# Kernel optimization log

Hardware: AMD Instinct MI355X
Metric: run time of the kernel (lower is better)

The kernel has to match this reference:

```python
import jax, jax.numpy as jnp
import numpy as np

B, S, C, H, D = 4, 2048, 512, 8, 64
EPS = 1e-5
SCALE = D ** -0.5


def layer_norm(x, w, b):
    m = jnp.mean(x, axis=-1, keepdims=True)
    v = jnp.var(x, axis=-1, keepdims=True)
    return (x - m) * jax.lax.rsqrt(v + EPS) * w + b


def setup_inputs() -> dict:
    key = jax.random.key(0)
    ks = jax.random.split(key, 7)
    s = 0.02
    return {
        "x": jax.random.normal(ks[0], (B, S, C), jnp.float32),
        "Wq": jax.random.normal(ks[1], (C, H * D), jnp.float32) * s,
        "Wk": jax.random.normal(ks[2], (C, H * D), jnp.float32) * s,
        "Wv": jax.random.normal(ks[3], (C, H * D), jnp.float32) * s,
        "Wo": jax.random.normal(ks[4], (H * D, C), jnp.float32) * s,
        "ln1_w": jnp.ones((C,), jnp.float32), "ln1_b": jnp.zeros((C,), jnp.float32),
        "ff_ln1_w": jnp.ones((C,), jnp.float32), "ff_ln1_b": jnp.zeros((C,), jnp.float32),
        "ff_w1": jax.random.normal(ks[5], (C, C), jnp.float32) * s, "ff_b1": jnp.zeros((C,), jnp.float32),
        "ff_ln2_w": jnp.ones((C,), jnp.float32), "ff_ln2_b": jnp.zeros((C,), jnp.float32),
        "ff_w2": jax.random.normal(ks[6], (C, C), jnp.float32) * s, "ff_b2": jnp.zeros((C,), jnp.float32),
        "ln2_w": jnp.ones((C,), jnp.float32), "ln2_b": jnp.zeros((C,), jnp.float32),
    }


def causal_attention(x, Wq, Wk, Wv, Wo):
    # Mathematically identical to the bucketed memory-efficient attention:
    # online-softmax bucketing changes compute order, not the result.
    q = (x @ Wq).reshape(B, S, H, D).transpose(0, 2, 1, 3)  # [B,H,S,D]
    k = (x @ Wk).reshape(B, S, H, D).transpose(0, 2, 1, 3)
    v = (x @ Wv).reshape(B, S, H, D).transpose(0, 2, 1, 3)
    scores = jnp.einsum('bhqd,bhkd->bhqk', q, k) * SCALE  # [B,H,S,S]
    causal = jnp.tril(jnp.ones((S, S), bool))
    scores = jnp.where(causal, scores, jnp.finfo(scores.dtype).min)
    attn = jax.nn.softmax(scores, axis=-1)
    out = jnp.einsum('bhqk,bhkd->bhqd', attn, v)
    out = out.transpose(0, 2, 1, 3).reshape(B, S, H * D)
    return out @ Wo


def reference(x, Wq, Wk, Wv, Wo, ln1_w, ln1_b, ff_ln1_w, ff_ln1_b, ff_w1, ff_b1,
              ff_ln2_w, ff_ln2_b, ff_w2, ff_b2, ln2_w, ln2_b):
    a = causal_attention(x, Wq, Wk, Wv, Wo)
    x_ln = layer_norm(a + x, ln1_w, ln1_b)
    h = layer_norm(x_ln, ff_ln1_w, ff_ln1_b) @ ff_w1 + ff_b1
    h = layer_norm(h, ff_ln2_w, ff_ln2_b) @ ff_w2 + ff_b2
    return layer_norm(h + x_ln, ln2_w, ln2_b)
```

## Files before the change

### kernel.cpp

```cpp
#include <hip/hip_runtime.h>

#define B_ 4
#define S_ 2048
#define C_ 512
#define H_ 8
#define D_ 64
#define M_ 8192

typedef short s8v __attribute__((ext_vector_type(8)));
typedef short s4v __attribute__((ext_vector_type(4)));
typedef float f4v __attribute__((ext_vector_type(4)));
typedef unsigned short u16;
typedef unsigned int u32;

__device__ __forceinline__ u16 f2b(float f) {
    u32 u = __builtin_bit_cast(u32, f);
    u = u + 0x7fffu + ((u >> 16) & 1u);
    return (u16)(u >> 16);
}

__device__ __forceinline__ void b2f8(const s8v v, float* f) {
    #pragma unroll
    for (int k = 0; k < 8; ++k)
        f[k] = __builtin_bit_cast(float, (u32)(u16)v[k] << 16);
}

__device__ __forceinline__ void gl2lds16(const void* g, void* l) {
    __builtin_amdgcn_global_load_lds(
        (const __attribute__((address_space(1))) void*)g,
        (__attribute__((address_space(3))) void*)l, 16, 0, 0);
}

__global__ __launch_bounds__(256) void prep_k(const float* __restrict__ x,
                                              u16* __restrict__ xb,
                                              const float* __restrict__ s0,
                                              const float* __restrict__ s1,
                                              const float* __restrict__ s2,
                                              const float* __restrict__ s3,
                                              const float* __restrict__ s4,
                                              const float* __restrict__ s5,
                                              u16* __restrict__ d0,
                                              u16* __restrict__ d1,
                                              u16* __restrict__ d2,
                                              u16* __restrict__ d3,
                                              u16* __restrict__ d4,
                                              u16* __restrict__ d5)
{
    __shared__ float t[32][33];
    const int bx = blockIdx.x;
    if (bx < 4096) {
        const int i = (bx * 256 + (int)threadIdx.x) * 4;
        const float4 v = *(const float4*)&x[i];
        ushort4 o;
        o.x = f2b(v.x); o.y = f2b(v.y); o.z = f2b(v.z); o.w = f2b(v.w);
        *(ushort4*)&xb[i] = o;
        return;
    }
    const int tb = bx - 4096;
    const int z = tb >> 8, rem = tb & 255;
    const float* W; u16* Wt;
    switch (z) {
        case 0: W = s0; Wt = d0; break;
        case 1: W = s1; Wt = d1; break;
        case 2: W = s2; Wt = d2; break;
        case 3: W = s3; Wt = d3; break;
        case 4: W = s4; Wt = d4; break;
        default: W = s5; Wt = d5; break;
    }
    const int tx = threadIdx.x & 31, ty = threadIdx.x >> 5;
    const int n0 = (rem & 15) * 32, k0 = (rem >> 4) * 32;
    #pragma unroll
    for (int i = 0; i < 4; ++i)
        t[ty + i * 8][tx] = W[(size_t)(k0 + ty + i * 8) * C_ + n0 + tx];
    __syncthreads();
    #pragma unroll
    for (int i = 0; i < 4; ++i)
        Wt[(size_t)(n0 + ty + i * 8) * C_ + k0 + tx] = f2b(t[tx][ty + i * 8]);
}

template <bool OB>
__global__ __launch_bounds__(256) void gemm_k(const u16* __restrict__ A,
                                              const u16* __restrict__ Bt,
                                              const float* __restrict__ bias,
                                              void* __restrict__ outv)
{
    __shared__ u16 As[2][128][64];
    __shared__ u16 Bs[2][64][64];
    const int tid = threadIdx.x;
    const int lane = tid & 63, w = tid >> 6;
    const int q4 = lane >> 4, l16 = lane & 15;
    const int wr = w >> 1, wc = w & 1;
    const int bm = blockIdx.x * 128, bn = blockIdx.y * 64;
    const int sr8  = lane >> 3;
    const int scol = ((lane & 7) ^ sr8) * 8;

    f4v acc[4][2];
    #pragma unroll
    for (int i = 0; i < 4; ++i)
        #pragma unroll
        for (int j = 0; j < 2; ++j) acc[i][j] = (f4v){0.f, 0.f, 0.f, 0.f};

    const u16* Ab = A  + (size_t)bm * C_;
    const u16* Bb = Bt + (size_t)bn * C_;

    auto stage = [&](int bf, int kt) {
        const int k0 = kt * 64;
        #pragma unroll
        for (int t = 0; t < 4; ++t)
            gl2lds16(Ab + (size_t)(w * 32 + t * 8 + sr8) * C_ + k0 + scol,
                     (char*)As + bf * 16384 + (w * 32 + t * 8) * 128);
        #pragma unroll
        for (int t = 0; t < 2; ++t)
            gl2lds16(Bb + (size_t)(w * 16 + t * 8 + sr8) * C_ + k0 + scol,
                     (char*)Bs + bf * 8192 + (w * 16 + t * 8) * 128);
    };

    stage(0, 0);
    for (int kt = 0; kt < 8; ++kt) {
        __syncthreads();
        const int bf = kt & 1;
        if (kt < 7) stage(bf ^ 1, kt + 1);
        #pragma unroll
        for (int kk = 0; kk < 2; ++kk) {
            const int pc = ((kk * 4 + q4) ^ (l16 & 7)) * 8;
            s8v a[4], b[2];
            #pragma unroll
            for (int i = 0; i < 4; ++i)
                a[i] = *(const s8v*)&As[bf][wr * 64 + i * 16 + l16][pc];
            #pragma unroll
            for (int j = 0; j < 2; ++j)
                b[j] = *(const s8v*)&Bs[bf][wc * 32 + j * 16 + l16][pc];
            #pragma unroll
            for (int i = 0; i < 4; ++i)
                #pragma unroll
                for (int j = 0; j < 2; ++j)
                    acc[i][j] = __builtin_amdgcn_mfma_f32_16x16x32_bf16(a[i], b[j], acc[i][j], 0, 0, 0);
        }
    }

    #pragma unroll
    for (int j = 0; j < 2; ++j) {
        const int n = bn + wc * 32 + j * 16 + l16;
        const float bj = bias ? bias[n] : 0.0f;
        #pragma unroll
        for (int i = 0; i < 4; ++i) {
            const int m = bm + wr * 64 + i * 16 + q4 * 4;
            #pragma unroll
            for (int reg = 0; reg < 4; ++reg) {
                const float vv = acc[i][j][reg] + bj;
                if constexpr (OB) ((u16*)outv)[(size_t)(m + reg) * C_ + n] = f2b(vv);
                else              ((float*)outv)[(size_t)(m + reg) * C_ + n] = vv;
            }
        }
    }
}

__global__ __launch_bounds__(256) void qkv_k(const u16* __restrict__ A,
                                             const u16* __restrict__ Wq,
                                             const u16* __restrict__ Wk,
                                             const u16* __restrict__ Wv,
                                             u16* __restrict__ oq,
                                             u16* __restrict__ ok,
                                             u16* __restrict__ ovt)
{
    __shared__ u16 As[2][128][64];
    __shared__ u16 Bs[2][64][64];
    const int tid = threadIdx.x;
    const int lane = tid & 63, w = tid >> 6;
    const int q4 = lane >> 4, l16 = lane & 15;
    const int wr = w >> 1, wc = w & 1;
    const int nt = blockIdx.y, which = nt >> 3;
    const u16* Bt = which == 0 ? Wq : (which == 1 ? Wk : Wv);
    const int bm = blockIdx.x * 128, bn = (nt & 7) * 64;
    const int sr8  = lane >> 3;
    const int scol = ((lane & 7) ^ sr8) * 8;

    f4v acc[4][2];
    #pragma unroll
    for (int i = 0; i < 4; ++i)
        #pragma unroll
        for (int j = 0; j < 2; ++j) acc[i][j] = (f4v){0.f, 0.f, 0.f, 0.f};

    const u16* Ab = A  + (size_t)bm * C_;
    const u16* Bb = Bt + (size_t)bn * C_;

    auto stage = [&](int bf, int kt) {
        const int k0 = kt * 64;
        #pragma unroll
        for (int t = 0; t < 4; ++t)
            gl2lds16(Ab + (size_t)(w * 32 + t * 8 + sr8) * C_ + k0 + scol,
                     (char*)As + bf * 16384 + (w * 32 + t * 8) * 128);
        #pragma unroll
        for (int t = 0; t < 2; ++t)
            gl2lds16(Bb + (size_t)(w * 16 + t * 8 + sr8) * C_ + k0 + scol,
                     (char*)Bs + bf * 8192 + (w * 16 + t * 8) * 128);
    };

    stage(0, 0);
    for (int kt = 0; kt < 8; ++kt) {
        __syncthreads();
        const int bf = kt & 1;
        if (kt < 7) stage(bf ^ 1, kt + 1);
        #pragma unroll
        for (int kk = 0; kk < 2; ++kk) {
            const int pc = ((kk * 4 + q4) ^ (l16 & 7)) * 8;
            s8v a[4], b[2];
            #pragma unroll
            for (int i = 0; i < 4; ++i)
                a[i] = *(const s8v*)&As[bf][wr * 64 + i * 16 + l16][pc];
            #pragma unroll
            for (int j = 0; j < 2; ++j)
                b[j] = *(const s8v*)&Bs[bf][wc * 32 + j * 16 + l16][pc];
            #pragma unroll
            for (int i = 0; i < 4; ++i)
                #pragma unroll
                for (int j = 0; j < 2; ++j)
                    acc[i][j] = __builtin_amdgcn_mfma_f32_16x16x32_bf16(a[i], b[j], acc[i][j], 0, 0, 0);
        }
    }

    if (which == 0) {
        #pragma unroll
        for (int j = 0; j < 2; ++j) {
            const int n = bn + wc * 32 + j * 16 + l16;
            #pragma unroll
            for (int i = 0; i < 4; ++i) {
                const int m = bm + wr * 64 + i * 16 + q4 * 4;
                #pragma unroll
                for (int reg = 0; reg < 4; ++reg)
                    oq[(size_t)(m + reg) * C_ + n] = f2b(acc[i][j][reg]);
            }
        }
    } else if (which == 1) {
        #pragma unroll
        for (int j = 0; j < 2; ++j) {
            const int n = bn + wc * 32 + j * 16 + l16;
            const int nswz = (n & ~31) | ((((n >> 3) & 3) ^ q4) << 3) | (n & 7);
            #pragma unroll
            for (int i = 0; i < 4; ++i) {
                const int m = bm + wr * 64 + i * 16 + q4 * 4;
                #pragma unroll
                for (int reg = 0; reg < 4; ++reg)
                    ok[(size_t)(m + reg) * C_ + nswz] = f2b(acc[i][j][reg]);
            }
        }
    } else {
        const int bglob = bm >> 11;
        const int sbase = bm & (S_ - 1);
        #pragma unroll
        for (int j = 0; j < 2; ++j) {
            const int n = bn + wc * 32 + j * 16 + l16;
            const int h = n >> 6, d = n & 63;
            u16* vrow = ovt + ((size_t)(bglob * H_ + h) * D_ + d) * S_;
            const int xw = d & 7;
            #pragma unroll
            for (int i = 0; i < 4; ++i) {
                const int s = sbase + wr * 64 + i * 16 + q4 * 4;
                const int pg = ((s & 31) >> 2) ^ xw;
                s4v pv;
                #pragma unroll
                for (int reg = 0; reg < 4; ++reg) pv[reg] = (short)f2b(acc[i][j][reg]);
                *(s4v*)&vrow[(s & ~31) + (pg << 2)] = pv;
            }
        }
    }
}

__global__ __launch_bounds__(256) void ln2xb_k(const u16* __restrict__ in,
                                               const float* __restrict__ res,
                                               const float* __restrict__ w1,
                                               const float* __restrict__ b1,
                                               const float* __restrict__ w2,
                                               const float* __restrict__ b2,
                                               u16* __restrict__ out1,
                                               u16* __restrict__ out2)
{
    const int lane = threadIdx.x & 63;
    const int row  = blockIdx.x * 4 + (threadIdx.x >> 6);
    const size_t off = (size_t)row * C_ + lane * 8;
    float v[8];
    b2f8(*(const s8v*)&in[off], v);
    {
        const float4 r0 = *(const float4*)&res[off];
        const float4 r1 = *(const float4*)&res[off + 4];
        v[0] += r0.x; v[1] += r0.y; v[2] += r0.z; v[3] += r0.w;
        v[4] += r1.x; v[5] += r1.y; v[6] += r1.z; v[7] += r1.w;
    }
    float s = 0.f, ss = 0.f;
    #pragma unroll
    for (int k = 0; k < 8; ++k) { s += v[k]; ss += v[k] * v[k]; }
    #pragma unroll
    for (int o = 32; o >= 1; o >>= 1) { s += __shfl_xor(s, o); ss += __shfl_xor(ss, o); }
    float mean = s * (1.0f / C_);
    float rstd = rsqrtf(ss * (1.0f / C_) - mean * mean + 1e-5f);

    const float4 wA0 = *(const float4*)&w1[lane * 8];
    const float4 wA1 = *(const float4*)&w1[lane * 8 + 4];
    const float4 bA0 = *(const float4*)&b1[lane * 8];
    const float4 bA1 = *(const float4*)&b1[lane * 8 + 4];
    const float wA[8] = {wA0.x, wA0.y, wA0.z, wA0.w, wA1.x, wA1.y, wA1.z, wA1.w};
    const float bA[8] = {bA0.x, bA0.y, bA0.z, bA0.w, bA1.x, bA1.y, bA1.z, bA1.w};
    float y[8];
    s8v o1;
    #pragma unroll
    for (int k = 0; k < 8; ++k) {
        y[k] = (v[k] - mean) * rstd * wA[k] + bA[k];
        o1[k] = (short)f2b(y[k]);
    }
    *(s8v*)&out1[off] = o1;

    s = 0.f; ss = 0.f;
    #pragma unroll
    for (int k = 0; k < 8; ++k) { s += y[k]; ss += y[k] * y[k]; }
    #pragma unroll
    for (int o = 32; o >= 1; o >>= 1) { s += __shfl_xor(s, o); ss += __shfl_xor(ss, o); }
    mean = s * (1.0f / C_);
    rstd = rsqrtf(ss * (1.0f / C_) - mean * mean + 1e-5f);

    const float4 wB0 = *(const float4*)&w2[lane * 8];
    const float4 wB1 = *(const float4*)&w2[lane * 8 + 4];
    const float4 bB0 = *(const float4*)&b2[lane * 8];
    const float4 bB1 = *(const float4*)&b2[lane * 8 + 4];
    const float wB[8] = {wB0.x, wB0.y, wB0.z, wB0.w, wB1.x, wB1.y, wB1.z, wB1.w};
    const float bB[8] = {bB0.x, bB0.y, bB0.z, bB0.w, bB1.x, bB1.y, bB1.z, bB1.w};
    s8v o2;
    #pragma unroll
    for (int k = 0; k < 8; ++k)
        o2[k] = (short)f2b((y[k] - mean) * rstd * wB[k] + bB[k]);
    *(s8v*)&out2[off] = o2;
}

__global__ __launch_bounds__(256) void lnb_k(const u16* __restrict__ in,
                                             const float* __restrict__ w,
                                             const float* __restrict__ bb,
                                             u16* __restrict__ out)
{
    const int lane = threadIdx.x & 63;
    const int row  = blockIdx.x * 4 + (threadIdx.x >> 6);
    const size_t off = (size_t)row * C_ + lane * 8;
    float v[8];
    b2f8(*(const s8v*)&in[off], v);
    float s = 0.f, ss = 0.f;
    #pragma unroll
    for (int k = 0; k < 8; ++k) { s += v[k]; ss += v[k] * v[k]; }
    #pragma unroll
    for (int o = 32; o >= 1; o >>= 1) { s += __shfl_xor(s, o); ss += __shfl_xor(ss, o); }
    const float mean = s * (1.0f / C_);
    const float rstd = rsqrtf(ss * (1.0f / C_) - mean * mean + 1e-5f);
    const float4 w0 = *(const float4*)&w[lane * 8];
    const float4 w1 = *(const float4*)&w[lane * 8 + 4];
    const float4 b0 = *(const float4*)&bb[lane * 8];
    const float4 b1 = *(const float4*)&bb[lane * 8 + 4];
    const float wv[8] = {w0.x, w0.y, w0.z, w0.w, w1.x, w1.y, w1.z, w1.w};
    const float bv[8] = {b0.x, b0.y, b0.z, b0.w, b1.x, b1.y, b1.z, b1.w};
    s8v o;
    #pragma unroll
    for (int k = 0; k < 8; ++k)
        o[k] = (short)f2b((v[k] - mean) * rstd * wv[k] + bv[k]);
    *(s8v*)&out[off] = o;
}

__global__ __launch_bounds__(256) void lnfin_k(const u16* __restrict__ in,
                                               const u16* __restrict__ res,
                                               const float* __restrict__ w,
                                               const float* __restrict__ bb,
                                               float* __restrict__ out)
{
    const int lane = threadIdx.x & 63;
    const int row  = blockIdx.x * 4 + (threadIdx.x >> 6);
    const size_t off = (size_t)row * C_ + lane * 8;
    float v[8], r[8];
    b2f8(*(const s8v*)&in[off], v);
    b2f8(*(const s8v*)&res[off], r);
    #pragma unroll
    for (int k = 0; k < 8; ++k) v[k] += r[k];
    float s = 0.f, ss = 0.f;
    #pragma unroll
    for (int k = 0; k < 8; ++k) { s += v[k]; ss += v[k] * v[k]; }
    #pragma unroll
    for (int o = 32; o >= 1; o >>= 1) { s += __shfl_xor(s, o); ss += __shfl_xor(ss, o); }
    const float mean = s * (1.0f / C_);
    const float rstd = rsqrtf(ss * (1.0f / C_) - mean * mean + 1e-5f);
    const float4 w0 = *(const float4*)&w[lane * 8];
    const float4 w1 = *(const float4*)&w[lane * 8 + 4];
    const float4 b0 = *(const float4*)&bb[lane * 8];
    const float4 b1 = *(const float4*)&bb[lane * 8 + 4];
    const float wv[8] = {w0.x, w0.y, w0.z, w0.w, w1.x, w1.y, w1.z, w1.w};
    const float bv[8] = {b0.x, b0.y, b0.z, b0.w, b1.x, b1.y, b1.z, b1.w};
    float4 o0, o1;
    o0.x = (v[0] - mean) * rstd * wv[0] + bv[0];
    o0.y = (v[1] - mean) * rstd * wv[1] + bv[1];
    o0.z = (v[2] - mean) * rstd * wv[2] + bv[2];
    o0.w = (v[3] - mean) * rstd * wv[3] + bv[3];
    o1.x = (v[4] - mean) * rstd * wv[4] + bv[4];
    o1.y = (v[5] - mean) * rstd * wv[5] + bv[5];
    o1.z = (v[6] - mean) * rstd * wv[6] + bv[6];
    o1.w = (v[7] - mean) * rstd * wv[7] + bv[7];
    *(float4*)&out[off]     = o0;
    *(float4*)&out[off + 4] = o1;
}

__global__ __launch_bounds__(512, 4) void attn_k(const u16* __restrict__ Q,
                                                 const u16* __restrict__ K,
                                                 const u16* __restrict__ Vt,
                                                 u16* __restrict__ O)
{
    __shared__ char smem[65536];
    u16* KsB = (u16*)smem;
    u16* VsB = (u16*)(smem + 32768);
    const int tid = threadIdx.x;
    const int lane = tid & 63, w = tid >> 6;
    const int grp = w >> 2, wl = w & 3;
    const int q4 = lane >> 4, l16 = lane & 15;
    const int h = blockIdx.y, b = blockIdx.z;
    const int px = blockIdx.x;
    const int qH = 31 - px, qL = px;
    const int nH = 32 - px;
    const size_t base  = ((size_t)b * S_) * C_ + h * D_;
    const size_t basev = ((size_t)(b * H_ + h)) * D_ * S_;
    const int lr = lane >> 2, lc = (lane & 3) * 8;
    const int kq = (q4 ^ ((l16 >> 2) & 3)) * 8;
    const int qrow = wl * 16 + l16;

    auto stage = [&](int kb, int sl) {
        #pragma unroll
        for (int r = 0; r < 2; ++r) {
            const int seg = r * 4 + wl;
            const int row = (seg & 3) * 16 + lr;
            const int kh = seg >> 2;
            gl2lds16(K  + base  + (size_t)(kb * 64 + row) * C_ + kh * 32 + lc,
                     (char*)KsB + sl * 8192 + seg * 1024);
            gl2lds16(Vt + basev + (size_t)row * S_ + kb * 64 + kh * 32 + lc,
                     (char*)VsB + sl * 8192 + seg * 1024);
        }
    };

    s8v qf[2];
    #pragma unroll
    for (int kh = 0; kh < 2; ++kh)
        qf[kh] = *(const s8v*)&Q[base + (size_t)(qH * 64 + qrow) * C_ + kh * 32 + q4 * 8];

    f4v acc[4]; float lp[4];
    f4v oH[4];  float lpH[4];
    #pragma unroll
    for (int j = 0; j < 4; ++j) {
        acc[j] = (f4v){0.f, 0.f, 0.f, 0.f}; lp[j] = 0.f;
        oH[j]  = (f4v){0.f, 0.f, 0.f, 0.f}; lpH[j] = 0.f;
    }
    bool dumped = false;

    stage(grp, grp);

    for (int t = 0; t <= 16; ++t) {
        __syncthreads();
        const int s = 2 * t + grp;
        if (s <= 32) {
            const int s2 = s + 2;
            if (s2 <= 32) {
                const int kb2 = s2 < nH ? s2 : s2 - nH;
                stage(kb2, s2 & 3);
            }
            if (s >= nH && !dumped) {
                dumped = true;
                #pragma unroll
                for (int j = 0; j < 4; ++j) {
                    oH[j] = acc[j]; lpH[j] = lp[j];
                    acc[j] = (f4v){0.f, 0.f, 0.f, 0.f}; lp[j] = 0.f;
                }
                #pragma unroll
                for (int kh = 0; kh < 2; ++kh)
                    qf[kh] = *(const s8v*)&Q[base + (size_t)(qL * 64 + qrow) * C_ + kh * 32 + q4 * 8];
            }
            const int kb = s < nH ? s : s - nH;
            const int sl = s & 3;
            const u16* ks = KsB + sl * 4096;
            const u16* vs = VsB + sl * 4096;

            f4v sc[4];
            #pragma unroll
            for (int j = 0; j < 4; ++j) sc[j] = (f4v){0.f, 0.f, 0.f, 0.f};
            __builtin_amdgcn_s_setprio(1);
            #pragma unroll
            for (int kh = 0; kh < 2; ++kh) {
                #pragma unroll
                for (int j = 0; j < 4; ++j) {
                    const s8v kf = *(const s8v*)&ks[(kh * 64 + j * 16 + l16) * 32 + kq];
                    sc[j] = __builtin_amdgcn_mfma_f32_16x16x32_bf16(kf, qf[kh], sc[j], 0, 0, 0);
                }
            }
            __builtin_amdgcn_s_setprio(0);

            s4v pa[4];
            const bool diag = (s == nH - 1) || (s == 32);
            if (diag) {
                #pragma unroll
                for (int j = 0; j < 4; ++j) {
                    float ps = 0.0f;
                    #pragma unroll
                    for (int reg = 0; reg < 4; ++reg) {
                        float tt = fmaf(sc[j][reg], 0.18033688011112043f, -11.541560327111707f);
                        if ((j * 16 + q4 * 4 + reg) > qrow) tt = -128.0f;
                        const float p = exp2f(tt);
                        ps += p;
                        pa[j][reg] = (short)(__builtin_bit_cast(u32, p) >> 16);
                    }
                    lp[j] += ps;
                }
            } else {
                #pragma unroll
                for (int j = 0; j < 4; ++j) {
                    float ps = 0.0f;
                    #pragma unroll
                    for (int reg = 0; reg < 4; ++reg) {
                        const float p = exp2f(fmaf(sc[j][reg], 0.18033688011112043f,
                                                   -11.541560327111707f));
                        ps += p;
                        pa[j][reg] = (short)(__builtin_bit_cast(u32, p) >> 16);
                    }
                    lp[j] += ps;
                }
            }

            __builtin_amdgcn_s_setprio(1);
            #pragma unroll
            for (int c = 0; c < 4; ++c) {
                const int gh = (((c & 1) * 4 + q4) ^ (l16 & 7)) * 4;
                #pragma unroll
                for (int dj = 0; dj < 4; ++dj) {
                    const s4v vb = *(const s4v*)&vs[((c >> 1) * 64 + dj * 16 + l16) * 32 + gh];
                    acc[dj] = __builtin_amdgcn_mfma_f32_16x16x16bf16_1k(pa[c], vb, acc[dj], 0, 0, 0);
                }
            }
            __builtin_amdgcn_s_setprio(0);
        }
    }

    if (!dumped) {
        #pragma unroll
        for (int j = 0; j < 4; ++j) {
            oH[j] = acc[j]; lpH[j] = lp[j];
            acc[j] = (f4v){0.f, 0.f, 0.f, 0.f}; lp[j] = 0.f;
        }
    }

    __syncthreads();
    float* exH = (float*)smem;
    float* exL = (float*)(smem + 20480);
    {
        float* p = (grp ? exH : exL) + (wl * 64 + lane) * 20;
        if (grp) {
            #pragma unroll
            for (int dj = 0; dj < 4; ++dj)
                #pragma unroll
                for (int reg = 0; reg < 4; ++reg) p[dj * 4 + reg] = oH[dj][reg];
            #pragma unroll
            for (int j = 0; j < 4; ++j) p[16 + j] = lpH[j];
        } else {
            #pragma unroll
            for (int dj = 0; dj < 4; ++dj)
                #pragma unroll
                for (int reg = 0; reg < 4; ++reg) p[dj * 4 + reg] = acc[dj][reg];
            #pragma unroll
            for (int j = 0; j < 4; ++j) p[16 + j] = lp[j];
        }
    }
    __syncthreads();
    if (grp == 0) {
        const float* p = exH + (wl * 64 + lane) * 20;
        #pragma unroll
        for (int dj = 0; dj < 4; ++dj)
            #pragma unroll
            for (int reg = 0; reg < 4; ++reg) oH[dj][reg] += p[dj * 4 + reg];
        #pragma unroll
        for (int j = 0; j < 4; ++j) lpH[j] += p[16 + j];
        float lt = (lpH[0] + lpH[1]) + (lpH[2] + lpH[3]);
        lt += __shfl_xor(lt, 16);
        lt += __shfl_xor(lt, 32);
        #pragma unroll
        for (int reg = 0; reg < 4; ++reg) {
            const float inv = 1.0f / __shfl(lt, q4 * 4 + reg);
            const size_t rowoff = base + (size_t)(qH * 64 + wl * 16 + q4 * 4 + reg) * C_;
            #pragma unroll
            for (int dj = 0; dj < 4; ++dj)
                O[rowoff + dj * 16 + l16] = f2b(oH[dj][reg] * inv);
        }
    } else {
        const float* p = exL + (wl * 64 + lane) * 20;
        #pragma unroll
        for (int dj = 0; dj < 4; ++dj)
            #pragma unroll
            for (int reg = 0; reg < 4; ++reg) acc[dj][reg] += p[dj * 4 + reg];
        #pragma unroll
        for (int j = 0; j < 4; ++j) lp[j] += p[16 + j];
        float lt = (lp[0] + lp[1]) + (lp[2] + lp[3]);
        lt += __shfl_xor(lt, 16);
        lt += __shfl_xor(lt, 32);
        #pragma unroll
        for (int reg = 0; reg < 4; ++reg) {
            const float inv = 1.0f / __shfl(lt, q4 * 4 + reg);
            const size_t rowoff = base + (size_t)(qL * 64 + wl * 16 + q4 * 4 + reg) * C_;
            #pragma unroll
            for (int dj = 0; dj < 4; ++dj)
                O[rowoff + dj * 16 + l16] = f2b(acc[dj][reg] * inv);
        }
    }
}

extern "C" void kernel_launch(void* const* d_in, const int* in_sizes, int n_in,
                              void* d_out, int out_size, void* d_ws, size_t ws_size,
                              hipStream_t stream)
{
    const float* x       = (const float*)d_in[0];
    const float* Wq      = (const float*)d_in[1];
    const float* Wk      = (const float*)d_in[2];
    const float* Wv      = (const float*)d_in[3];
    const float* Wo      = (const float*)d_in[4];
    const float* ln1_w   = (const float*)d_in[5];
    const float* ln1_b   = (const float*)d_in[6];
    const float* ffln1_w = (const float*)d_in[7];
    const float* ffln1_b = (const float*)d_in[8];
    const float* ff_w1   = (const float*)d_in[9];
    const float* ff_b1   = (const float*)d_in[10];
    const float* ffln2_w = (const float*)d_in[11];
    const float* ffln2_b = (const float*)d_in[12];
    const float* ff_w2   = (const float*)d_in[13];
    const float* ff_b2   = (const float*)d_in[14];
    const float* ln2_w   = (const float*)d_in[15];
    const float* ln2_b   = (const float*)d_in[16];
    float* out = (float*)d_out;

    const size_t MC = (size_t)M_ * C_;
    const size_t WW = (size_t)C_ * C_;
    u16* xb   = (u16*)d_ws;
    u16* WqT  = xb + MC;
    u16* WkT  = WqT + WW;
    u16* WvT  = WkT + WW;
    u16* WoT  = WvT + WW;
    u16* W1T  = WoT + WW;
    u16* W2T  = W1T + WW;
    u16* qbuf = W2T + WW;
    u16* kbuf = qbuf + MC;
    u16* vbuf = kbuf + MC;
    u16* vtbuf= vbuf + MC;
    u16*  abuf = xb;
    u16*  tf   = qbuf;
    u16*  xln  = vbuf;

    const dim3 gg(M_ / 128, C_ / 64);
    const dim3 gq(M_ / 128, 24);
    const dim3 ga(16, H_, B_);
    const int  gl = M_ / 4;

    prep_k<<<5632, 256, 0, stream>>>(x, xb, Wq, Wk, Wv, Wo, ff_w1, ff_w2,
                                     WqT, WkT, WvT, WoT, W1T, W2T);

    qkv_k<<<gq, 256, 0, stream>>>(xb, WqT, WkT, WvT, qbuf, kbuf, vtbuf);
    attn_k<<<ga, 512, 0, stream>>>(qbuf, kbuf, vtbuf, abuf);

    gemm_k<true><<<gg, 256, 0, stream>>>(abuf, WoT, nullptr, tf);
    ln2xb_k<<<gl, 256, 0, stream>>>(tf, x, ln1_w, ln1_b, ffln1_w, ffln1_b,
                                    xln, xb);
    gemm_k<true><<<gg, 256, 0, stream>>>(xb, W1T, ff_b1, tf);
    lnb_k<<<gl, 256, 0, stream>>>(tf, ffln2_w, ffln2_b, xb);
    gemm_k<true><<<gg, 256, 0, stream>>>(xb, W2T, ff_b2, tf);
    lnfin_k<<<gl, 256, 0, stream>>>(tf, xln, ln2_w, ln2_b, out);
}
```

Before: 230.5 us.

## Unroll attention loop into ping-pong LDS stages with incremental pointers and swapped grid order

Restructures the attention main loop into a two-stage unrolled ping-pong over fixed LDS buffers. Global-to-LDS addresses are now advanced incrementally, with a single wrap at the high/low boundary, instead of recomputing slot and block indices every step, and the per-lane fragment offsets are precomputed. The grid is reordered so the head index is fastest-varying, which changes how blocks sharing a batch are scheduled and how they reuse L2. This cuts scalar and index overhead and branches in the inner loop, at the cost of more complex control flow and code size.

```diff
diff --git a/kernel.cpp b/kernel.cpp
--- a/kernel.cpp
+++ b/kernel.cpp
@@ -412,8 +412,7 @@
     const int lane = tid & 63, w = tid >> 6;
     const int grp = w >> 2, wl = w & 3;
     const int q4 = lane >> 4, l16 = lane & 15;
-    const int h = blockIdx.y, b = blockIdx.z;
-    const int px = blockIdx.x;
+    const int h = blockIdx.x, px = blockIdx.y, b = blockIdx.z;
     const int qH = 31 - px, qL = px;
     const int nH = 32 - px;
     const size_t base  = ((size_t)b * S_) * C_ + h * D_;
@@ -422,23 +421,23 @@
     const int kq = (q4 ^ ((l16 >> 2) & 3)) * 8;
     const int qrow = wl * 16 + l16;
 
-    auto stage = [&](int kb, int sl) {
-        #pragma unroll
-        for (int r = 0; r < 2; ++r) {
-            const int seg = r * 4 + wl;
-            const int row = (seg & 3) * 16 + lr;
-            const int kh = seg >> 2;
-            gl2lds16(K  + base  + (size_t)(kb * 64 + row) * C_ + kh * 32 + lc,
-                     (char*)KsB + sl * 8192 + seg * 1024);
-            gl2lds16(Vt + basev + (size_t)row * S_ + kb * 64 + kh * 32 + lc,
-                     (char*)VsB + sl * 8192 + seg * 1024);
-        }
-    };
-
-    s8v qf[2];
-    #pragma unroll
-    for (int kh = 0; kh < 2; ++kh)
-        qf[kh] = *(const s8v*)&Q[base + (size_t)(qH * 64 + qrow) * C_ + kh * 32 + q4 * 8];
+    const u16* ksA = KsB + grp * 4096;
+    const u16* ksBp = KsB + (grp + 2) * 4096;
+    const u16* vsA = VsB + grp * 4096;
+    const u16* vsBp = VsB + (grp + 2) * 4096;
+    char* kdA = (char*)KsB + grp * 8192 + wl * 1024;
+    char* kdB = (char*)KsB + (grp + 2) * 8192 + wl * 1024;
+    char* vdA = (char*)VsB + grp * 8192 + wl * 1024;
+    char* vdB = (char*)VsB + (grp + 2) * 8192 + wl * 1024;
+
+    const int kfb = l16 * 32 + kq;
+    int vfb[4];
+    #pragma unroll
+    for (int c = 0; c < 4; ++c)
+        vfb[c] = l16 * 32 + ((((c & 1) * 4 + q4) ^ (l16 & 7)) * 4);
+
+    const u16* kpt = K  + base  + (size_t)(wl * 16 + lr) * C_ + lc;
+    const u16* vpt = Vt + basev + (size_t)(wl * 16 + lr) * S_ + lc;
 
     f4v acc[4]; float lp[4];
     f4v oH[4];  float lpH[4];
@@ -447,94 +446,124 @@
         acc[j] = (f4v){0.f, 0.f, 0.f, 0.f}; lp[j] = 0.f;
         oH[j]  = (f4v){0.f, 0.f, 0.f, 0.f}; lpH[j] = 0.f;
     }
-    bool dumped = false;
-
-    stage(grp, grp);
-
-    for (int t = 0; t <= 16; ++t) {
+    s8v qf[2];
+    #pragma unroll
+    for (int kh = 0; kh < 2; ++kh)
+        qf[kh] = *(const s8v*)&Q[base + (size_t)(qH * 64 + qrow) * C_ + kh * 32 + q4 * 8];
+
+    bool dumped = false, wrapped = false;
+
+    auto dumpacc = [&]() {
+        #pragma unroll
+        for (int j = 0; j < 4; ++j) {
+            oH[j] = acc[j]; lpH[j] = lp[j];
+            acc[j] = (f4v){0.f, 0.f, 0.f, 0.f}; lp[j] = 0.f;
+        }
+        #pragma unroll
+        for (int kh = 0; kh < 2; ++kh)
+            qf[kh] = *(const s8v*)&Q[base + (size_t)(qL * 64 + qrow) * C_ + kh * 32 + q4 * 8];
+    };
+
+    auto compute = [&](const u16* ks, const u16* vs, const bool diag) {
+        f4v sc[4];
+        #pragma unroll
+        for (int j = 0; j < 4; ++j) sc[j] = (f4v){0.f, 0.f, 0.f, 0.f};
+        __builtin_amdgcn_s_setprio(1);
+        #pragma unroll
+        for (int kh = 0; kh < 2; ++kh)
+            #pragma unroll
+            for (int j = 0; j < 4; ++j) {
+                const s8v kf = *(const s8v*)&ks[kfb + kh * 2048 + j * 512];
+                sc[j] = __builtin_amdgcn_mfma_f32_16x16x32_bf16(kf, qf[kh], sc[j], 0, 0, 0);
+            }
+        __builtin_amdgcn_s_setprio(0);
+        s4v pa[4];
+        if (diag) {
+            #pragma unroll
+            for (int j = 0; j < 4; ++j) {
+                float ps = 0.0f;
+                #pragma unroll
+                for (int reg = 0; reg < 4; ++reg) {
+                    float tt = fmaf(sc[j][reg], 0.18033688011112043f, -11.541560327111707f);
+                    if ((j * 16 + q4 * 4 + reg) > qrow) tt = -128.0f;
+                    const float p = exp2f(tt);
+                    ps += p;
+                    pa[j][reg] = (short)(__builtin_bit_cast(u32, p) >> 16);
+                }
+                lp[j] += ps;
+            }
+        } else {
+            #pragma unroll
+            for (int j = 0; j < 4; ++j) {
+                float ps = 0.0f;
+                #pragma unroll
+                for (int reg = 0; reg < 4; ++reg) {
+                    const float p = exp2f(fmaf(sc[j][reg], 0.18033688011112043f,
+                                               -11.541560327111707f));
+                    ps += p;
+                    pa[j][reg] = (short)(__builtin_bit_cast(u32, p) >> 16);
+                }
+                lp[j] += ps;
+            }
+        }
+        __builtin_amdgcn_s_setprio(1);
+        #pragma unroll
+        for (int c = 0; c < 4; ++c)
+            #pragma unroll
+            for (int dj = 0; dj < 4; ++dj) {
+                const s4v vb = *(const s4v*)&vs[vfb[c] + (c >> 1) * 2048 + dj * 512];
+                acc[dj] = __builtin_amdgcn_mfma_f32_16x16x16bf16_1k(pa[c], vb, acc[dj], 0, 0, 0);
+            }
+        __builtin_amdgcn_s_setprio(0);
+    };
+
+    {
+        const u16* kc = kpt + (size_t)(grp * 64) * C_;
+        const u16* vc = vpt + grp * 64;
+        gl2lds16(kc, kdA); gl2lds16(kc + 32, kdA + 4096);
+        gl2lds16(vc, vdA); gl2lds16(vc + 32, vdA + 4096);
+    }
+    const u16* kcur = kpt + (size_t)((grp + 2) * 64) * C_;
+    const u16* vcur = vpt + (grp + 2) * 64;
+    int snext = grp + 2;
+    int s = grp;
+
+    auto advance = [&]() {
+        kcur += (size_t)128 * C_;
+        vcur += 128;
+        snext += 2;
+        if (!wrapped && snext >= nH) {
+            kcur -= (size_t)(nH * 64) * C_;
+            vcur -= nH * 64;
+            wrapped = true;
+        }
+    };
+
+    for (int u = 0; u < 8; ++u) {
         __syncthreads();
-        const int s = 2 * t + grp;
-        if (s <= 32) {
-            const int s2 = s + 2;
-            if (s2 <= 32) {
-                const int kb2 = s2 < nH ? s2 : s2 - nH;
-                stage(kb2, s2 & 3);
-            }
-            if (s >= nH && !dumped) {
-                dumped = true;
-                #pragma unroll
-                for (int j = 0; j < 4; ++j) {
-                    oH[j] = acc[j]; lpH[j] = lp[j];
-                    acc[j] = (f4v){0.f, 0.f, 0.f, 0.f}; lp[j] = 0.f;
-                }
-                #pragma unroll
-                for (int kh = 0; kh < 2; ++kh)
-                    qf[kh] = *(const s8v*)&Q[base + (size_t)(qL * 64 + qrow) * C_ + kh * 32 + q4 * 8];
-            }
-            const int kb = s < nH ? s : s - nH;
-            const int sl = s & 3;
-            const u16* ks = KsB + sl * 4096;
-            const u16* vs = VsB + sl * 4096;
-
-            f4v sc[4];
-            #pragma unroll
-            for (int j = 0; j < 4; ++j) sc[j] = (f4v){0.f, 0.f, 0.f, 0.f};
-            __builtin_amdgcn_s_setprio(1);
-            #pragma unroll
-            for (int kh = 0; kh < 2; ++kh) {
-                #pragma unroll
-                for (int j = 0; j < 4; ++j) {
-                    const s8v kf = *(const s8v*)&ks[(kh * 64 + j * 16 + l16) * 32 + kq];
-                    sc[j] = __builtin_amdgcn_mfma_f32_16x16x32_bf16(kf, qf[kh], sc[j], 0, 0, 0);
-                }
-            }
-            __builtin_amdgcn_s_setprio(0);
-
-            s4v pa[4];
-            const bool diag = (s == nH - 1) || (s == 32);
-            if (diag) {
-                #pragma unroll
-                for (int j = 0; j < 4; ++j) {
-                    float ps = 0.0f;
-                    #pragma unroll
-                    for (int reg = 0; reg < 4; ++reg) {
-                        float tt = fmaf(sc[j][reg], 0.18033688011112043f, -11.541560327111707f);
-                        if ((j * 16 + q4 * 4 + reg) > qrow) tt = -128.0f;
-                        const float p = exp2f(tt);
-                        ps += p;
-                        pa[j][reg] = (short)(__builtin_bit_cast(u32, p) >> 16);
-                    }
-                    lp[j] += ps;
-                }
-            } else {
-                #pragma unroll
-                for (int j = 0; j < 4; ++j) {
-                    float ps = 0.0f;
-                    #pragma unroll
-                    for (int reg = 0; reg < 4; ++reg) {
-                        const float p = exp2f(fmaf(sc[j][reg], 0.18033688011112043f,
-                                                   -11.541560327111707f));
-                        ps += p;
-                        pa[j][reg] = (short)(__builtin_bit_cast(u32, p) >> 16);
-                    }
-                    lp[j] += ps;
-                }
-            }
-
-            __builtin_amdgcn_s_setprio(1);
-            #pragma unroll
-            for (int c = 0; c < 4; ++c) {
-                const int gh = (((c & 1) * 4 + q4) ^ (l16 & 7)) * 4;
-                #pragma unroll
-                for (int dj = 0; dj < 4; ++dj) {
-                    const s4v vb = *(const s4v*)&vs[((c >> 1) * 64 + dj * 16 + l16) * 32 + gh];
-                    acc[dj] = __builtin_amdgcn_mfma_f32_16x16x16bf16_1k(pa[c], vb, acc[dj], 0, 0, 0);
-                }
-            }
-            __builtin_amdgcn_s_setprio(0);
-        }
-    }
-
+        {
+            gl2lds16(kcur, kdB); gl2lds16(kcur + 32, kdB + 4096);
+            gl2lds16(vcur, vdB); gl2lds16(vcur + 32, vdB + 4096);
+            advance();
+        }
+        if (!dumped && s >= nH) { dumped = true; dumpacc(); }
+        compute(ksA, vsA, (s == nH - 1) || (s == 32));
+        s += 2;
+        __syncthreads();
+        if (u < 7 || grp == 0) {
+            gl2lds16(kcur, kdA); gl2lds16(kcur + 32, kdA + 4096);
+            gl2lds16(vcur, vdA); gl2lds16(vcur + 32, vdA + 4096);
+            advance();
+        }
+        if (!dumped && s >= nH) { dumped = true; dumpacc(); }
+        compute(ksBp, vsBp, (s == nH - 1) || (s == 32));
+        s += 2;
+    }
+    __syncthreads();
+    if (grp == 0) {
+        if (!dumped) { dumped = true; dumpacc(); }
+        compute(ksA, vsA, true);
+    }
     if (!dumped) {
         #pragma unroll
         for (int j = 0; j < 4; ++j) {
@@ -648,7 +677,7 @@
 
     const dim3 gg(M_ / 128, C_ / 64);
     const dim3 gq(M_ / 128, 24);
-    const dim3 ga(16, H_, B_);
+    const dim3 ga(H_, 16, B_);
     const int  gl = M_ / 4;
 
     prep_k<<<5632, 256, 0, stream>>>(x, xb, Wq, Wk, Wv, Wo, ff_w1, ff_w2,
```

Measured after the change: 220.2 us. -4.5%, faster.
